# Kernel optimization log

Measured on AMD Instinct MI355X. Metric: run time of the kernel, lower is better.

The kernel has to match this reference:

```python
import jax, jax.numpy as jnp
import numpy as np

B, HID = 32768, 64


def setup_inputs() -> dict:
    key = jax.random.key(0)
    ks = jax.random.split(key, 16)
    N = 128
    inp = {
        "z": jax.random.normal(ks[0], (B, 2), jnp.float32),
        "u": jax.random.uniform(ks[1], (B, 2, N - 1), jnp.float32),
        "w0_1": jax.random.normal(ks[2], (HID, 1), jnp.float32) * 0.5,
        "b0_1": jax.random.normal(ks[3], (HID,), jnp.float32) * 0.1,
        "w0_2": jax.random.normal(ks[4], (HID, HID), jnp.float32) * (1.0 / np.sqrt(HID)),
        "b0_2": jax.random.normal(ks[5], (HID,), jnp.float32) * 0.1,
        "w0_3": jax.random.normal(ks[6], (1, HID), jnp.float32) * (1.0 / np.sqrt(HID)),
        "b0_3": jax.random.normal(ks[7], (1,), jnp.float32) * 0.1,
        "w1_1": jax.random.normal(ks[8], (HID, 1), jnp.float32) * 0.5,
        "b1_1": jax.random.normal(ks[9], (HID,), jnp.float32) * 0.1,
        "w1_2": jax.random.normal(ks[10], (HID, HID), jnp.float32) * (1.0 / np.sqrt(HID)),
        "b1_2": jax.random.normal(ks[11], (HID,), jnp.float32) * 0.1,
        "w1_3": jax.random.normal(ks[12], (1, HID), jnp.float32) * (1.0 / np.sqrt(HID)),
        "b1_3": jax.random.normal(ks[13], (1,), jnp.float32) * 0.1,
        "bias": jax.random.uniform(ks[14], (1,), jnp.float32),
        "N": N,
        "lower_bound": -5,
    }
    return inp


def _mlp(x, w1, b1, w2, b2, w3, b3):
    # x: (B, N) scalar inputs; 1 -> HID -> HID -> 1 with LeakyReLU(0.01), final ELU
    h = jax.nn.leaky_relu(x[..., None] * w1[:, 0] + b1, 0.01)          # (B, N, HID)
    h = jax.nn.leaky_relu(jnp.einsum("bnh,kh->bnk", h, w2) + b2, 0.01)  # (B, N, HID)
    o = jax.nn.elu(jnp.einsum("bnk,k->bn", h, w3[0]) + b3[0])           # (B, N)
    return o


def reference(z, u, w0_1, b0_1, w0_2, b0_2, w0_3, b0_3,
              w1_1, b1_1, w1_2, b1_2, w1_3, b1_3, bias, N, lower_bound):
    lb = jnp.asarray(lower_bound, z.dtype)
    zc = jnp.clip(z, lb, None)                         # clamp(min=lower_bound)
    d_size = (zc - lb) / jnp.asarray(N - 1, z.dtype)   # (B, 2)
    grid = jnp.arange(N, dtype=z.dtype)                # (N,)
    z_split = d_size[:, :, None] * grid + lb           # (B, 2, N)
    # jitter: U(0, d_size) for first N-1 bins, 0 for the last bin
    zeros_last = jnp.zeros(z_split.shape[:2] + (1,), z.dtype)
    z_random = z_split + jnp.concatenate([u * d_size[:, :, None], zeros_last], axis=-1)
    out0 = _mlp(z_random[:, 0, :], w0_1, b0_1, w0_2, b0_2, w0_3, b0_3)  # (B, N)
    out1 = _mlp(z_random[:, 1, :], w1_1, b1_1, w1_2, b1_2, w1_3, b1_3)  # (B, N)
    Hz0 = ((out0 + 1.0) * d_size[:, 0:1]).sum(axis=1)  # (B,)
    Hz1 = ((out1 + 1.0) * d_size[:, 1:2]).sum(axis=1)  # (B,)
    return Hz0 + Hz1 + bias[0]                         # (B,)
```

## Files before the change

### kernel.cpp

```cpp
#include <hip/hip_runtime.h>

#define NT 2048
#define XMAX 8.0f


__device__ __forceinline__ float wave_sum_lane63(float v) {
#define DPP_ADD(ctrl)                                                         \
    v += __int_as_float(__builtin_amdgcn_update_dpp(                          \
        0, __float_as_int(v), (ctrl), 0xf, 0xf, false))
    DPP_ADD(0x111);
    DPP_ADD(0x112);
    DPP_ADD(0x114);
    DPP_ADD(0x118);
    DPP_ADD(0x142);
    DPP_ADD(0x143);
#undef DPP_ADD
    return v;
}

#define W2STRIDE 76

__global__ __launch_bounds__(256) void build_table(
    const float* __restrict__ w01, const float* __restrict__ b01,
    const float* __restrict__ w02, const float* __restrict__ b02,
    const float* __restrict__ w03, const float* __restrict__ b03,
    const float* __restrict__ w11, const float* __restrict__ b11,
    const float* __restrict__ w12, const float* __restrict__ b12,
    const float* __restrict__ w13, const float* __restrict__ b13,
    const int* __restrict__ lbp, float* __restrict__ T)
{
    __shared__ float W2s[64 * W2STRIDE];
    __shared__ float w1s[64], b1s[64], b2s[64], w3s[64];

    const int tid = threadIdx.x;
    const int d  = blockIdx.x & 1;
    const int e0 = (blockIdx.x >> 1) * 16;

    const float* w1p = d ? w11 : w01;
    const float* b1p = d ? b11 : b01;
    const float* w2p = d ? w12 : w02;
    const float* b2p = d ? b12 : b02;
    const float* w3p = d ? w13 : w03;
    const float  b3  = (d ? b13 : b03)[0];

    #pragma unroll
    for (int j = 0; j < 16; ++j) {
        const int idx = tid + 256 * j;
        W2s[(idx >> 6) * W2STRIDE + (idx & 63)] = w2p[idx];
    }
    if (tid < 64) {
        w1s[tid] = w1p[tid];
        b1s[tid] = b1p[tid];
        b2s[tid] = b2p[tid];
        w3s[tid] = w3p[tid];
    }
    __syncthreads();

    const int e   = e0 + (tid >> 4);
    const int sub = tid & 15;

    const float lb = (float)lbp[0];
    const float delta = (XMAX - lb) / (float)(NT - 1);
    const float x = fmaf((float)e, delta, lb);

    float h1[64];
    #pragma unroll
    for (int k = 0; k < 64; ++k) {
        const float t = fmaf(x, w1s[k], b1s[k]);
        h1[k] = fmaxf(t, 0.01f * t);
    }

    float s = 0.0f;
    #pragma unroll
    for (int ff = 0; ff < 4; ++ff) {
        const int f = (sub << 2) + ff;
        const float4* row = (const float4*)&W2s[f * W2STRIDE];
        float a = b2s[f];
        #pragma unroll
        for (int k4 = 0; k4 < 16; ++k4) {
            const float4 w = row[k4];
            a = fmaf(w.x, h1[4 * k4 + 0], a);
            a = fmaf(w.y, h1[4 * k4 + 1], a);
            a = fmaf(w.z, h1[4 * k4 + 2], a);
            a = fmaf(w.w, h1[4 * k4 + 3], a);
        }
        s = fmaf(fmaxf(a, 0.01f * a), w3s[f], s);
    }

    s += __shfl_xor(s, 1);
    s += __shfl_xor(s, 2);
    s += __shfl_xor(s, 4);
    s += __shfl_xor(s, 8);
    if (sub == 0) T[d * NT + e] = s + b3;
}

__global__ __launch_bounds__(256) void integrate_tab(
    const float* __restrict__ zin, const float* __restrict__ uin,
    const float* __restrict__ Tg, const int* __restrict__ lbp,
    const float* __restrict__ biasp, float* __restrict__ out)
{
    __shared__ float Ts[2][NT];
    __shared__ float lds_hz[4][8];

    const int tid  = threadIdx.x;
    const int lane = tid & 63;
    const int wave = tid >> 6;
    const int d    = wave & 1;
    const int bg   = wave >> 1;
    const int b0 = blockIdx.x * 16 + bg * 8;

    const float lb = (float)lbp[0];
    const float scale = (float)(NT - 1) / (XMAX - lb);
    const float biasv = biasp[0];

    #pragma unroll
    for (int j = 0; j < 2 * NT / 256; ++j)
        ((float*)Ts)[tid + j * 256] = Tg[tid + j * 256];
    __syncthreads();

    const float* Td = Ts[d];
    const float n0 = (float)(2 * lane);
    const float n1 = (float)(2 * lane + 1);
    const bool last = (lane == 63);

    float z_n = zin[b0 * 2 + d];
    float2 u_n;
    {
        const float* ub = uin + (size_t)(b0 * 2 + d) * 127;
        u_n.x = ub[2 * lane];
        u_n.y = last ? 0.0f : ub[2 * lane + 1];
    }

    #pragma unroll 1
    for (int i = 0; i < 8; ++i) {
        const float zv = z_n;
        const float2 uu = u_n;

        const int bn = b0 + ((i < 7) ? i + 1 : 7);
        z_n = zin[bn * 2 + d];
        {
            const float* ub = uin + (size_t)(bn * 2 + d) * 127;
            u_n.x = ub[2 * lane];
            u_n.y = last ? 0.0f : ub[2 * lane + 1];
        }

        const float ds  = (fmaxf(zv, lb) - lb) * (1.0f / 127.0f);
        const float dsc = ds * scale;
        const float t0 = (n0 + uu.x) * dsc;
        const float t1 = (n1 + uu.y) * dsc;

        int i0 = (int)t0; i0 = min(i0, NT - 2);
        int i1 = (int)t1; i1 = min(i1, NT - 2);
        const float f0 = t0 - (float)i0;
        const float f1 = t1 - (float)i1;

        const float a0 = Td[i0], a0b = Td[i0 + 1];
        const float a1 = Td[i1], a1b = Td[i1 + 1];
        const float s0 = fmaf(f0, a0b - a0, a0);
        const float s1 = fmaf(f1, a1b - a1, a1);

        const float e0 = __builtin_amdgcn_exp2f(s0 * 1.4426950408889634f);
        const float e1 = __builtin_amdgcn_exp2f(s1 * 1.4426950408889634f);
        float acc = ((s0 > 0.0f) ? (s0 + 1.0f) : e0)
                  + ((s1 > 0.0f) ? (s1 + 1.0f) : e1);

        acc = wave_sum_lane63(acc);

        if (lane == 63) lds_hz[wave][i] = acc * ds;
    }

    __syncthreads();
    if (tid < 16) {
        const int g = tid >> 3, l = tid & 7;
        out[blockIdx.x * 16 + g * 8 + l] = lds_hz[2 * g][l] + lds_hz[2 * g + 1][l] + biasv;
    }
}

extern "C" void kernel_launch(void* const* d_in, const int* in_sizes, int n_in,
                              void* d_out, int out_size, void* d_ws, size_t ws_size,
                              hipStream_t stream) {
    const float* z    = (const float*)d_in[0];
    const float* u    = (const float*)d_in[1];
    const float* w0_1 = (const float*)d_in[2];
    const float* b0_1 = (const float*)d_in[3];
    const float* w0_2 = (const float*)d_in[4];
    const float* b0_2 = (const float*)d_in[5];
    const float* w0_3 = (const float*)d_in[6];
    const float* b0_3 = (const float*)d_in[7];
    const float* w1_1 = (const float*)d_in[8];
    const float* b1_1 = (const float*)d_in[9];
    const float* w1_2 = (const float*)d_in[10];
    const float* b1_2 = (const float*)d_in[11];
    const float* w1_3 = (const float*)d_in[12];
    const float* b1_3 = (const float*)d_in[13];
    const float* bias = (const float*)d_in[14];
    const int*   lbp  = (const int*)d_in[16];

    float* T = (float*)d_ws;

    build_table<<<dim3(256), dim3(256), 0, stream>>>(
        w0_1, b0_1, w0_2, b0_2, w0_3, b0_3,
        w1_1, b1_1, w1_2, b1_2, w1_3, b1_3,
        lbp, T);

    integrate_tab<<<dim3(2048), dim3(256), 0, stream>>>(z, u, T, lbp, bias, (float*)d_out);
}
```

Before: 112.6 us.

## Map 8 lanes per batch row and issue all u loads before table staging

Restructures the integrate kernel so each wave handles 8 batch rows at once, with 8 lanes per row each processing 16 bins, instead of looping serially over 8 rows with 64 lanes each. All u loads are issued up front, before the table is copied to LDS, and that copy now uses float4. The full 64-lane DPP reduction becomes a 3-step reduction within 8-lane groups. This removes the serial per-row loop and its six-step reductions and overlaps global loads with the LDS staging, at the cost of more registers and strided u loads (each lane reads with stride 8).

```diff
diff --git a/kernel.cpp b/kernel.cpp
--- a/kernel.cpp
+++ b/kernel.cpp
@@ -3,20 +3,6 @@
 #define NT 2048
 #define XMAX 8.0f
 
-
-__device__ __forceinline__ float wave_sum_lane63(float v) {
-#define DPP_ADD(ctrl)                                                         \
-    v += __int_as_float(__builtin_amdgcn_update_dpp(                          \
-        0, __float_as_int(v), (ctrl), 0xf, 0xf, false))
-    DPP_ADD(0x111);
-    DPP_ADD(0x112);
-    DPP_ADD(0x114);
-    DPP_ADD(0x118);
-    DPP_ADD(0x142);
-    DPP_ADD(0x143);
-#undef DPP_ADD
-    return v;
-}
 
 #define W2STRIDE 76
 
@@ -107,67 +93,60 @@
     const int wave = tid >> 6;
     const int d    = wave & 1;
     const int bg   = wave >> 1;
-    const int b0 = blockIdx.x * 16 + bg * 8;
+    const int b0   = blockIdx.x * 16 + bg * 8;
+
+    const int bb = lane >> 3;
+    const int p  = lane & 7;
+    const int b  = b0 + bb;
 
     const float lb = (float)lbp[0];
     const float scale = (float)(NT - 1) / (XMAX - lb);
     const float biasv = biasp[0];
 
+    const float zv = zin[b * 2 + d];
+    const float* ub = uin + (size_t)(b * 2 + d) * 127;
+    float uv[16];
     #pragma unroll
-    for (int j = 0; j < 2 * NT / 256; ++j)
-        ((float*)Ts)[tid + j * 256] = Tg[tid + j * 256];
+    for (int j = 0; j < 16; ++j) {
+        const int n = 8 * j + p;
+        uv[j] = (n < 127) ? ub[n] : 0.0f;
+    }
+
+    const float4* Tg4 = (const float4*)Tg;
+    float4* Ts4 = (float4*)Ts;
+    #pragma unroll
+    for (int j = 0; j < (2 * NT) / (4 * 256); ++j)
+        Ts4[tid + j * 256] = Tg4[tid + j * 256];
     __syncthreads();
 
     const float* Td = Ts[d];
-    const float n0 = (float)(2 * lane);
-    const float n1 = (float)(2 * lane + 1);
-    const bool last = (lane == 63);
 
-    float z_n = zin[b0 * 2 + d];
-    float2 u_n;
-    {
-        const float* ub = uin + (size_t)(b0 * 2 + d) * 127;
-        u_n.x = ub[2 * lane];
-        u_n.y = last ? 0.0f : ub[2 * lane + 1];
+    const float ds  = (fmaxf(zv, lb) - lb) * (1.0f / 127.0f);
+    const float dsc = ds * scale;
+
+    float acc = 0.0f;
+    #pragma unroll
+    for (int j = 0; j < 16; ++j) {
+        const float nf = (float)(8 * j + p);
+        const float t  = (nf + uv[j]) * dsc;
+        int i0 = (int)t;
+        i0 = min(i0, NT - 2);
+        const float f0 = t - (float)i0;
+        const float a0 = Td[i0], a1 = Td[i0 + 1];
+        const float s0 = fmaf(f0, a1 - a0, a0);
+        const float e0 = __builtin_amdgcn_exp2f(s0 * 1.4426950408889634f);
+        acc += (s0 > 0.0f) ? (s0 + 1.0f) : e0;
     }
 
-    #pragma unroll 1
-    for (int i = 0; i < 8; ++i) {
-        const float zv = z_n;
-        const float2 uu = u_n;
+#define DPP_ADD(ctrl)                                                         \
+    acc += __int_as_float(__builtin_amdgcn_update_dpp(                        \
+        0, __float_as_int(acc), (ctrl), 0xf, 0xf, false))
+    DPP_ADD(0x111);
+    DPP_ADD(0x112);
+    DPP_ADD(0x114);
+#undef DPP_ADD
 
-        const int bn = b0 + ((i < 7) ? i + 1 : 7);
-        z_n = zin[bn * 2 + d];
-        {
-            const float* ub = uin + (size_t)(bn * 2 + d) * 127;
-            u_n.x = ub[2 * lane];
-            u_n.y = last ? 0.0f : ub[2 * lane + 1];
-        }
-
-        const float ds  = (fmaxf(zv, lb) - lb) * (1.0f / 127.0f);
-        const float dsc = ds * scale;
-        const float t0 = (n0 + uu.x) * dsc;
-        const float t1 = (n1 + uu.y) * dsc;
-
-        int i0 = (int)t0; i0 = min(i0, NT - 2);
-        int i1 = (int)t1; i1 = min(i1, NT - 2);
-        const float f0 = t0 - (float)i0;
-        const float f1 = t1 - (float)i1;
-
-        const float a0 = Td[i0], a0b = Td[i0 + 1];
-        const float a1 = Td[i1], a1b = Td[i1 + 1];
-        const float s0 = fmaf(f0, a0b - a0, a0);
-        const float s1 = fmaf(f1, a1b - a1, a1);
-
-        const float e0 = __builtin_amdgcn_exp2f(s0 * 1.4426950408889634f);
-        const float e1 = __builtin_amdgcn_exp2f(s1 * 1.4426950408889634f);
-        float acc = ((s0 > 0.0f) ? (s0 + 1.0f) : e0)
-                  + ((s1 > 0.0f) ? (s1 + 1.0f) : e1);
-
-        acc = wave_sum_lane63(acc);
-
-        if (lane == 63) lds_hz[wave][i] = acc * ds;
-    }
+    if (p == 7) lds_hz[wave][bb] = acc * ds;
 
     __syncthreads();
     if (tid < 16) {
```

Result: no change. 113.3 us (+0.6%).
